# Kernel tuning notes

Measured on AMD Instinct MI355X. Metric: run time of the kernel, lower is better.

## Reference

```python
import jax, jax.numpy as jnp
import numpy as np
import math

D_MODEL = 1024
NUM_HEADS = 16
HEAD_DIM = D_MODEL // NUM_HEADS


def _xavier(key, out_f, in_f):
    limit = math.sqrt(6.0 / (in_f + out_f))
    return jax.random.uniform(key, (out_f, in_f), jnp.float32, -limit, limit)


def ternarize(w):
    # abs-mean threshold -> {-1, 0, +1}
    abs_mean = jnp.mean(jnp.abs(w))
    return jnp.where(jnp.abs(w) > abs_mean, jnp.sign(w), jnp.zeros_like(w))


def setup_inputs() -> dict:
    key = jax.random.key(0)
    kq, kk, kv, kwq, kwk, kwv, kwo = jax.random.split(key, 7)
    B, S = 2, 2048
    return {
        "query": jax.random.normal(kq, (B, S, D_MODEL), jnp.float32),
        "key": jax.random.normal(kk, (B, S, D_MODEL), jnp.float32),
        "value": jax.random.normal(kv, (B, S, D_MODEL), jnp.float32),
        "w_q": _xavier(kwq, D_MODEL, D_MODEL),
        "w_k": _xavier(kwk, D_MODEL, D_MODEL),
        "w_v": _xavier(kwv, D_MODEL, D_MODEL),
        "w_o": _xavier(kwo, D_MODEL, D_MODEL),
    }


def reference(query, key, value, w_q, w_k, w_v, w_o):
    B, S, _ = query.shape
    # ternary projections (F.linear: x @ W.T)
    q = query @ ternarize(w_q).T
    k = key @ ternarize(w_k).T
    v = value @ ternarize(w_v).T
    # [B, H, S, Dh]
    q = q.reshape(B, S, NUM_HEADS, HEAD_DIM).transpose(0, 2, 1, 3)
    k = k.reshape(B, -1, NUM_HEADS, HEAD_DIM).transpose(0, 2, 1, 3)
    v = v.reshape(B, -1, NUM_HEADS, HEAD_DIM).transpose(0, 2, 1, 3)
    scores = jnp.einsum("bhqd,bhkd->bhqk", q, k) / math.sqrt(HEAD_DIM)
    probs = jax.nn.softmax(scores, axis=-1)
    out = jnp.einsum("bhqk,bhkd->bhqd", probs, v)
    out = out.transpose(0, 2, 1, 3).reshape(B, S, D_MODEL)
    return out @ ternarize(w_o).T
```

## Files before the change

kernel.cpp:

```cpp
#include <hip/hip_runtime.h>
#include <cstdint>
#include <cstddef>

typedef __bf16 bfloat;
typedef __bf16 bf16x8 __attribute__((ext_vector_type(8)));
typedef __bf16 bf16x4 __attribute__((ext_vector_type(4)));
typedef float  f32x4  __attribute__((ext_vector_type(4)));

static constexpr int D  = 1024;
static constexpr int S  = 2048;
static constexpr int B  = 2;
static constexpr int H  = 16;
static constexpr int DH = 64;
static constexpr int M  = B * S;
static constexpr int WMAT_N = 1024 * 1024;

#define MFMA_BF16(a, b, c) __builtin_amdgcn_mfma_f32_16x16x32_bf16((a), (b), (c), 0, 0, 0)

__device__ __forceinline__ void gl_lds16(const void* g, void* l) {
  __builtin_amdgcn_global_load_lds(
      (const __attribute__((address_space(1))) void*)g,
      (__attribute__((address_space(3))) void*)l, 16, 0, 0);
}

__global__ void prep_kernel(const float* __restrict__ w0, const float* __restrict__ w1,
                            const float* __restrict__ w2, const float* __restrict__ w3,
                            double* __restrict__ sums) {
  const int y = blockIdx.y;
  const float* w = (y == 0) ? w0 : (y == 1) ? w1 : (y == 2) ? w2 : w3;
  const float4* w4 = (const float4*)w;
  double s = 0.0;
  for (int i = blockIdx.x * blockDim.x + threadIdx.x; i < (WMAT_N / 4);
       i += gridDim.x * blockDim.x) {
    float4 v = w4[i];
    s += (double)fabsf(v.x) + (double)fabsf(v.y) + (double)fabsf(v.z) + (double)fabsf(v.w);
  }
  for (int off = 1; off < 64; off <<= 1) s += __shfl_xor(s, off, 64);
  __shared__ double ps[4];
  if ((threadIdx.x & 63) == 0) ps[threadIdx.x >> 6] = s;
  __syncthreads();
  if (threadIdx.x == 0) atomicAdd(&sums[y], ps[0] + ps[1] + ps[2] + ps[3]);
}

__global__ void tern_kernel(const float* __restrict__ w0, const float* __restrict__ w1,
                            const float* __restrict__ w2, const float* __restrict__ w3,
                            bfloat* __restrict__ o0, bfloat* __restrict__ o1,
                            bfloat* __restrict__ o2, bfloat* __restrict__ o3,
                            const double* __restrict__ sums) {
  int z = blockIdx.y;
  const float* w = (z == 0) ? w0 : (z == 1) ? w1 : (z == 2) ? w2 : w3;
  bfloat* o = (z == 0) ? o0 : (z == 1) ? o1 : (z == 2) ? o2 : o3;
  double thr = sums[z] * (1.0 / (double)WMAT_N);
  const float4* w4 = (const float4*)w;
  for (int i = blockIdx.x * blockDim.x + threadIdx.x; i < (WMAT_N / 4);
       i += gridDim.x * blockDim.x) {
    float4 v = w4[i];
    bf16x4 r;
    r[0] = (bfloat)(((double)fabsf(v.x) > thr) ? (v.x > 0.f ? 1.f : -1.f) : 0.f);
    r[1] = (bfloat)(((double)fabsf(v.y) > thr) ? (v.y > 0.f ? 1.f : -1.f) : 0.f);
    r[2] = (bfloat)(((double)fabsf(v.z) > thr) ? (v.z > 0.f ? 1.f : -1.f) : 0.f);
    r[3] = (bfloat)(((double)fabsf(v.w) > thr) ? (v.w > 0.f ? 1.f : -1.f) : 0.f);
    *(bf16x4*)&o[(size_t)i * 4] = r;
  }
}

__global__ __launch_bounds__(256) void qkv_gemm(
    const float* __restrict__ xq, const float* __restrict__ xk,
    const float* __restrict__ xv, const bfloat* __restrict__ wqt,
    const bfloat* __restrict__ wkt, const bfloat* __restrict__ wvt,
    bfloat* __restrict__ qmh, bfloat* __restrict__ qml,
    bfloat* __restrict__ kmh, bfloat* __restrict__ kml, bfloat* __restrict__ vtr) {
  constexpr int K = D;
  constexpr int N = D;
  __shared__ __align__(16) bfloat As0[128 * 64];
  __shared__ __align__(16) bfloat As1[128 * 64];
  __shared__ __align__(16) bfloat Ws[128 * 64];

  const int bid = blockIdx.x;
  const int xcd = bid & 7;
  const int i6 = bid >> 3;
  const int slice = xcd * 12 + (i6 >> 3);
  const int bx = i6 & 7;
  const int z = slice >> 5;
  const int by = slice & 31;

  const float* Af;
  const bfloat* Wm;
  bfloat *Oh = nullptr, *Ol = nullptr;
  float scale = 1.f;
  bool split;
  if (z == 0) {
    Af = xq; Wm = wqt; Oh = qmh; Ol = qml;
    scale = 0.18033688f;
    split = true;
  } else if (z == 1) {
    Af = xk; Wm = wkt; Oh = kmh; Ol = kml; split = true;
  } else {
    Af = xv; Wm = wvt; split = false;
  }

  const int t = threadIdx.x;
  const int w = t >> 6, lane = t & 63;
  const int quad = lane >> 4, l16 = lane & 15;
  const int wm = w >> 1, wn = w & 1;
  const int m0 = by * 128, n0 = bx * 128;

  f32x4 acc[4][4] = {};

  const int srr = lane >> 3;
  const int spc = lane & 7;
  const int cl8 = (spc ^ srr) * 8;

  const float* aSrc[4];
#pragma unroll
  for (int g = 0; g < 4; g++)
    aSrc[g] = Af + (size_t)(m0 + w * 32 + g * 8 + srr) * K + cl8;

  float4 fa[4][2];
#pragma unroll
  for (int g = 0; g < 4; g++) {
    fa[g][0] = *(const float4*)(aSrc[g]);
    fa[g][1] = *(const float4*)(aSrc[g] + 4);
  }

  for (int kk = 0; kk < K; kk += 64) {
#pragma unroll
    for (int g = 0; g < 4; g++) {
      int rb = w * 32 + g * 8;
      gl_lds16(Wm + (size_t)(n0 + rb + srr) * K + kk + cl8, Ws + rb * 64);
    }
#pragma unroll
    for (int g = 0; g < 4; g++) {
      int row = w * 32 + g * 8 + srr;
      float f[8] = {fa[g][0].x, fa[g][0].y, fa[g][0].z, fa[g][0].w,
                    fa[g][1].x, fa[g][1].y, fa[g][1].z, fa[g][1].w};
      bf16x8 hh;
#pragma unroll
      for (int j = 0; j < 8; j++) hh[j] = (bfloat)f[j];
      const int da = row * 64 + spc * 8;
      *(bf16x8*)&As0[da] = hh;
      if (split) {
        bf16x8 ll;
#pragma unroll
        for (int j = 0; j < 8; j++) ll[j] = (bfloat)(f[j] - (float)hh[j]);
        *(bf16x8*)&As1[da] = ll;
      }
    }
    asm volatile("s_waitcnt vmcnt(0) lgkmcnt(0)" ::: "memory");
    __builtin_amdgcn_s_barrier();
    asm volatile("" ::: "memory");

    if (kk + 64 < K) {
#pragma unroll
      for (int g = 0; g < 4; g++) {
        fa[g][0] = *(const float4*)(aSrc[g] + kk + 64);
        fa[g][1] = *(const float4*)(aSrc[g] + kk + 64 + 4);
      }
    }

#pragma unroll
    for (int kidx = 0; kidx < 2; kidx++) {
      bf16x8 bfrag[4], afrag[4];
#pragma unroll
      for (int nt = 0; nt < 4; nt++) {
        int r = wn * 64 + nt * 16 + l16;
        bfrag[nt] = *(const bf16x8*)&Ws[r * 64 + (((kidx * 4 + quad) ^ (r & 7)) * 8)];
      }
#pragma unroll
      for (int mt = 0; mt < 4; mt++) {
        int r = wm * 64 + mt * 16 + l16;
        afrag[mt] = *(const bf16x8*)&As0[r * 64 + (((kidx * 4 + quad) ^ (r & 7)) * 8)];
      }
#pragma unroll
      for (int mt = 0; mt < 4; mt++)
#pragma unroll
        for (int nt = 0; nt < 4; nt++)
          acc[mt][nt] = MFMA_BF16(afrag[mt], bfrag[nt], acc[mt][nt]);
      if (split) {
#pragma unroll
        for (int mt = 0; mt < 4; mt++) {
          int r = wm * 64 + mt * 16 + l16;
          afrag[mt] = *(const bf16x8*)&As1[r * 64 + (((kidx * 4 + quad) ^ (r & 7)) * 8)];
        }
#pragma unroll
        for (int mt = 0; mt < 4; mt++)
#pragma unroll
          for (int nt = 0; nt < 4; nt++)
            acc[mt][nt] = MFMA_BF16(afrag[mt], bfrag[nt], acc[mt][nt]);
      }
    }
    asm volatile("" ::: "memory");
    __builtin_amdgcn_s_barrier();
    asm volatile("" ::: "memory");
  }

#pragma unroll
  for (int mt = 0; mt < 4; mt++) {
#pragma unroll
    for (int nt = 0; nt < 4; nt++) {
      const int row = m0 + wm * 64 + mt * 16 + quad * 4;
      const int col = n0 + wn * 64 + nt * 16 + l16;
      if (split) {
#pragma unroll
        for (int rg = 0; rg < 4; rg++) {
          float vv = acc[mt][nt][rg] * scale;
          size_t idx = (size_t)(row + rg) * N + col;
          bfloat hh = (bfloat)vv;
          Oh[idx] = hh;
          Ol[idx] = (bfloat)(vv - (float)hh);
        }
      } else {
        int bb = row >> 11, s = row & (S - 1);
        int kk6 = s & 63;
        int pos = (kk6 & 3) | (((kk6 >> 4) & 1) << 2) | (((kk6 >> 2) & 3) << 3) |
                  ((kk6 >> 5) << 5);
        int sp = (s & ~63) | pos;
        bf16x4 pk;
#pragma unroll
        for (int rg = 0; rg < 4; rg++) pk[rg] = (bfloat)acc[mt][nt][rg];
        *(bf16x4*)&vtr[(size_t)bb * D * S + (size_t)col * S + sp] = pk;
      }
    }
  }
}

__global__ __launch_bounds__(256) void gemm_wo(const bfloat* __restrict__ A,
                                               const bfloat* __restrict__ Wm,
                                               float* __restrict__ Cf) {
  constexpr int K = D;
  constexpr int N = D;
  __shared__ __align__(16) bfloat As[128 * 64];
  __shared__ __align__(16) bfloat Ws[64 * 64];

  const int bid = blockIdx.x;
  const int xcd = bid & 7;
  const int i6 = bid >> 3;
  const int by = xcd * 4 + (i6 >> 4);
  const int bx = i6 & 15;

  const int t = threadIdx.x;
  const int w = t >> 6, lane = t & 63;
  const int quad = lane >> 4, l16 = lane & 15;
  const int wm = w >> 1, wn = w & 1;
  const int m0 = by * 128, n0 = bx * 64;

  f32x4 acc[4][2] = {};

  const int srr = lane >> 3;
  const int spc = lane & 7;
  const int cl8 = (spc ^ srr) * 8;

  for (int kk = 0; kk < K; kk += 64) {
#pragma unroll
    for (int g = 0; g < 4; g++) {
      int rb = w * 32 + g * 8;
      gl_lds16(A + (size_t)(m0 + rb + srr) * K + kk + cl8, As + rb * 64);
    }
#pragma unroll
    for (int g = 0; g < 2; g++) {
      int rb = w * 16 + g * 8;
      gl_lds16(Wm + (size_t)(n0 + rb + srr) * K + kk + cl8, Ws + rb * 64);
    }
    __syncthreads();

#pragma unroll
    for (int kidx = 0; kidx < 2; kidx++) {
      bf16x8 af[4], bfr[2];
#pragma unroll
      for (int nt = 0; nt < 2; nt++) {
        int r = wn * 32 + nt * 16 + l16;
        bfr[nt] = *(const bf16x8*)&Ws[r * 64 + (((kidx * 4 + quad) ^ (r & 7)) * 8)];
      }
#pragma unroll
      for (int mt = 0; mt < 4; mt++) {
        int r = wm * 64 + mt * 16 + l16;
        af[mt] = *(const bf16x8*)&As[r * 64 + (((kidx * 4 + quad) ^ (r & 7)) * 8)];
      }
#pragma unroll
      for (int mt = 0; mt < 4; mt++)
#pragma unroll
        for (int nt = 0; nt < 2; nt++)
          acc[mt][nt] = MFMA_BF16(af[mt], bfr[nt], acc[mt][nt]);
    }
    __syncthreads();
  }

#pragma unroll
  for (int mt = 0; mt < 4; mt++) {
#pragma unroll
    for (int nt = 0; nt < 2; nt++) {
      const int row = m0 + wm * 64 + mt * 16 + quad * 4;
      const int col = n0 + wn * 32 + nt * 16 + l16;
#pragma unroll
      for (int rg = 0; rg < 4; rg++) Cf[(size_t)(row + rg) * N + col] = acc[mt][nt][rg];
    }
  }
}

__global__ __launch_bounds__(512) void flash_kernel(
    const bfloat* __restrict__ qh, const bfloat* __restrict__ ql,
    const bfloat* __restrict__ kh, const bfloat* __restrict__ kl,
    const bfloat* __restrict__ vt, bfloat* __restrict__ outp) {
  __shared__ __align__(16) bfloat SM[20480];

  const int tid = threadIdx.x;
  const int w = tid >> 6, lane = tid & 63;
  const int quad = lane >> 4, l16 = lane & 15;

  const int blk = blockIdx.x;
  const int xcd = blk & 7, slot = blk >> 3;
  const int g = xcd * 4 + (slot >> 4);
  const int h = g & 15, b = g >> 4;
  const int q0 = (slot & 15) * 128;

  const size_t base = (size_t)b * S * D + (size_t)h * DH;
  const size_t vbase = (size_t)b * D * S + (size_t)h * DH * S;

  const int ssr = lane >> 3;
  const int spc = lane & 7;
  const int c8 = (spc ^ ssr) * 8;
  const int stKV = w * 512;

  const bfloat* pKh = kh + base + (size_t)(w * 8 + ssr) * D + c8;
  const bfloat* pKl = kl + base + (size_t)(w * 8 + ssr) * D + c8;
  const bfloat* pV = vt + vbase + (size_t)(w * 8 + ssr) * S + c8;

  bf16x8 ones;
#pragma unroll
  for (int j = 0; j < 8; j++) ones[j] = (bfloat)1.f;

  {
    const bfloat* pQh = qh + base + (size_t)(q0 + w * 16 + ssr) * D + c8;
    const bfloat* pQl = ql + base + (size_t)(q0 + w * 16 + ssr) * D + c8;
    gl_lds16(pQh, SM + w * 1024);
    gl_lds16(pQh + 8 * D, SM + w * 1024 + 512);
    gl_lds16(pQl, SM + 8192 + w * 1024);
    gl_lds16(pQl + 8 * D, SM + 8192 + w * 1024 + 512);
  }
  asm volatile("s_waitcnt vmcnt(0)" ::: "memory");
  __builtin_amdgcn_s_barrier();
  asm volatile("" ::: "memory");

  const int fo0 = l16 * 64 + ((quad ^ (l16 & 7)) * 8);
  const int fo4 = fo0 ^ 32;
  const int fq = w * 1024;

  bf16x8 qhf0 = *(const bf16x8*)&SM[fq + fo0];
  bf16x8 qhf1 = *(const bf16x8*)&SM[fq + fo4];
  bf16x8 qlf0 = *(const bf16x8*)&SM[8192 + fq + fo0];
  bf16x8 qlf1 = *(const bf16x8*)&SM[8192 + fq + fo4];
  asm volatile("s_waitcnt lgkmcnt(0)" ::: "memory");
  __builtin_amdgcn_s_barrier();
  asm volatile("" ::: "memory");

  gl_lds16(pKh, SM + 0 + stKV);
  gl_lds16(pKl, SM + 4096 + stKV);
  pKh += 64 * D;
  pKl += 64 * D;
  asm volatile("s_waitcnt vmcnt(0)" ::: "memory");

  f32x4 Oa[4] = {};
  f32x4 La = {};
  float m_i = -3.0e38f;
  constexpr int NT = S / 64;

  for (int t = 0; t < NT; ++t) {
    __builtin_amdgcn_s_barrier();
    asm volatile("" ::: "memory");
    const int cur = (t & 1) * 8192;
    const int nxt = 8192 - cur;

    gl_lds16(pV, SM + 16384 + stKV);
    pV += 64;
    if (t < NT - 1) {
      gl_lds16(pKh, SM + nxt + stKV);
      gl_lds16(pKl, SM + nxt + 4096 + stKV);
      pKh += 64 * D;
      pKl += 64 * D;
    }

    f32x4 sf[4];
    __builtin_amdgcn_s_setprio(1);
#pragma unroll
    for (int mt = 0; mt < 4; mt++) {
      f32x4 a = {};
      bf16x8 bh0 = *(const bf16x8*)&SM[cur + fo0 + mt * 1024];
      bf16x8 bl0 = *(const bf16x8*)&SM[cur + 4096 + fo0 + mt * 1024];
      bf16x8 bh1 = *(const bf16x8*)&SM[cur + fo4 + mt * 1024];
      bf16x8 bl1 = *(const bf16x8*)&SM[cur + 4096 + fo4 + mt * 1024];
      a = MFMA_BF16(bh0, qhf0, a);
      a = MFMA_BF16(bl0, qhf0, a);
      a = MFMA_BF16(bh0, qlf0, a);
      a = MFMA_BF16(bh1, qhf1, a);
      a = MFMA_BF16(bl1, qhf1, a);
      a = MFMA_BF16(bh1, qlf1, a);
      sf[mt] = a;
    }
    __builtin_amdgcn_s_setprio(0);

    float t0 = fmaxf(fmaxf(sf[0][0], sf[0][1]), fmaxf(sf[0][2], sf[0][3]));
    float t1 = fmaxf(fmaxf(sf[1][0], sf[1][1]), fmaxf(sf[1][2], sf[1][3]));
    float t2 = fmaxf(fmaxf(sf[2][0], sf[2][1]), fmaxf(sf[2][2], sf[2][3]));
    float t3 = fmaxf(fmaxf(sf[3][0], sf[3][1]), fmaxf(sf[3][2], sf[3][3]));
    float mm = fmaxf(fmaxf(t0, t1), fmaxf(t2, t3));
    mm = fmaxf(mm, __shfl_xor(mm, 16, 64));
    mm = fmaxf(mm, __shfl_xor(mm, 32, 64));
    if (__ballot(mm > m_i + 8.0f)) {
      float mnew = fmaxf(m_i, mm);
      float alpha = exp2f(m_i - mnew);
      m_i = mnew;
#pragma unroll
      for (int mt = 0; mt < 4; mt++) Oa[mt] *= alpha;
      La *= alpha;
    }
#pragma unroll
    for (int mt = 0; mt < 4; mt++)
#pragma unroll
      for (int rg = 0; rg < 4; rg++) sf[mt][rg] = exp2f(sf[mt][rg] - m_i);

    if (t < NT - 1)
      asm volatile("s_waitcnt vmcnt(2)" ::: "memory");
    else
      asm volatile("s_waitcnt vmcnt(0)" ::: "memory");
    __builtin_amdgcn_s_barrier();
    asm volatile("" ::: "memory");

    __builtin_amdgcn_s_setprio(1);
#pragma unroll
    for (int kp = 0; kp < 2; kp++) {
      bf16x8 pb8;
#pragma unroll
      for (int rg = 0; rg < 4; rg++) {
        pb8[rg] = (bfloat)sf[2 * kp][rg];
        pb8[4 + rg] = (bfloat)sf[2 * kp + 1][rg];
      }
      La = MFMA_BF16(ones, pb8, La);
      const int fv = kp ? fo4 : fo0;
#pragma unroll
      for (int mt = 0; mt < 4; mt++) {
        bf16x8 va = *(const bf16x8*)&SM[16384 + fv + mt * 1024];
        Oa[mt] = MFMA_BF16(va, pb8, Oa[mt]);
      }
    }
    __builtin_amdgcn_s_setprio(0);
    asm volatile("s_waitcnt vmcnt(0)" ::: "memory");
  }

  float inv = 1.0f / La[0];
  const int qrow = q0 + w * 16 + l16;
#pragma unroll
  for (int mt = 0; mt < 4; mt++) {
    bf16x4 ov;
#pragma unroll
    for (int rg = 0; rg < 4; rg++) ov[rg] = (bfloat)(Oa[mt][rg] * inv);
    *(bf16x4*)&outp[base + (size_t)qrow * D + mt * 16 + quad * 4] = ov;
  }
}

extern "C" void kernel_launch(void* const* d_in, const int* in_sizes, int n_in,
                              void* d_out, int out_size, void* d_ws, size_t ws_size,
                              hipStream_t stream) {
  const float* q_in = (const float*)d_in[0];
  const float* k_in = (const float*)d_in[1];
  const float* v_in = (const float*)d_in[2];
  const float* wq = (const float*)d_in[3];
  const float* wk = (const float*)d_in[4];
  const float* wv = (const float*)d_in[5];
  const float* wo = (const float*)d_in[6];
  float* outp = (float*)d_out;
  char* ws = (char*)d_ws;

  constexpr size_t WBYTES = (size_t)WMAT_N * 2;
  constexpr size_t XBYTES = (size_t)M * D * 2;
  size_t off = 0;
  double* sums = (double*)(ws + off); off += 256;
  bfloat* wqt = (bfloat*)(ws + off); off += WBYTES;
  bfloat* wkt = (bfloat*)(ws + off); off += WBYTES;
  bfloat* wvt = (bfloat*)(ws + off); off += WBYTES;
  bfloat* wot = (bfloat*)(ws + off); off += WBYTES;
  bfloat* qmh = (bfloat*)(ws + off); off += XBYTES;
  bfloat* qml = (bfloat*)(ws + off); off += XBYTES;
  bfloat* kmh = (bfloat*)(ws + off); off += XBYTES;
  bfloat* kml = (bfloat*)(ws + off); off += XBYTES;
  bfloat* vtr = (bfloat*)(ws + off); off += XBYTES;
  bfloat* attn = (bfloat*)(ws + off); off += XBYTES;

  hipMemsetAsync(sums, 0, 4 * sizeof(double), stream);
  prep_kernel<<<dim3(256, 4), 256, 0, stream>>>(wq, wk, wv, wo, sums);
  tern_kernel<<<dim3(128, 4), 256, 0, stream>>>(wq, wk, wv, wo, wqt, wkt, wvt, wot, sums);
  qkv_gemm<<<768, 256, 0, stream>>>(
      q_in, k_in, v_in, wqt, wkt, wvt, qmh, qml, kmh, kml, vtr);
  flash_kernel<<<512, 512, 0, stream>>>(qmh, qml, kmh, kml, vtr, attn);
  gemm_wo<<<512, 256, 0, stream>>>(attn, wot, outp);
}
```

Baseline: 269.2 us.

## Load A fragments directly into registers and double-buffer weight tiles in LDS

The QKV projection GEMM no longer stages the fp32 activations through LDS as hi/lo bf16 tiles. Each lane now loads its MFMA A-fragment straight from global memory, converts it to hi/lo bf16 in registers, and prefetches the next k-step's fragment. The weight tile is double-buffered in LDS so the next tile's global-to-LDS load overlaps compute, which drops one barrier per iteration. In exchange the global A loads are less coalesced (per-lane 32-byte row chunks) and register pressure rises from holding two k-slices of fp32 prefetch.

```diff
diff --git a/kernel.cpp b/kernel.cpp
--- a/kernel.cpp
+++ b/kernel.cpp
@@ -72,9 +72,7 @@
     bfloat* __restrict__ kmh, bfloat* __restrict__ kml, bfloat* __restrict__ vtr) {
   constexpr int K = D;
   constexpr int N = D;
-  __shared__ __align__(16) bfloat As0[128 * 64];
-  __shared__ __align__(16) bfloat As1[128 * 64];
-  __shared__ __align__(16) bfloat Ws[128 * 64];
+  __shared__ __align__(16) bfloat Ws[2][128 * 64];
 
   const int bid = blockIdx.x;
   const int xcd = bid & 7;
@@ -111,87 +109,83 @@
   const int spc = lane & 7;
   const int cl8 = (spc ^ srr) * 8;
 
-  const float* aSrc[4];
+  const float* aB[4];
+#pragma unroll
+  for (int mt = 0; mt < 4; mt++)
+    aB[mt] = Af + (size_t)(m0 + wm * 64 + mt * 16 + l16) * K + quad * 8;
+
+  const bfloat* wB[4];
 #pragma unroll
   for (int g = 0; g < 4; g++)
-    aSrc[g] = Af + (size_t)(m0 + w * 32 + g * 8 + srr) * K + cl8;
-
-  float4 fa[4][2];
-#pragma unroll
-  for (int g = 0; g < 4; g++) {
-    fa[g][0] = *(const float4*)(aSrc[g]);
-    fa[g][1] = *(const float4*)(aSrc[g] + 4);
-  }
+    wB[g] = Wm + (size_t)(n0 + w * 32 + g * 8 + srr) * K + cl8;
+
+#pragma unroll
+  for (int g = 0; g < 4; g++) gl_lds16(wB[g], &Ws[0][(w * 32 + g * 8) * 64]);
+  float4 fa[4][2][2];
+#pragma unroll
+  for (int mt = 0; mt < 4; mt++)
+#pragma unroll
+    for (int kidx = 0; kidx < 2; kidx++) {
+      fa[mt][kidx][0] = *(const float4*)(aB[mt] + kidx * 32);
+      fa[mt][kidx][1] = *(const float4*)(aB[mt] + kidx * 32 + 4);
+    }
 
   for (int kk = 0; kk < K; kk += 64) {
-#pragma unroll
-    for (int g = 0; g < 4; g++) {
-      int rb = w * 32 + g * 8;
-      gl_lds16(Wm + (size_t)(n0 + rb + srr) * K + kk + cl8, Ws + rb * 64);
-    }
-#pragma unroll
-    for (int g = 0; g < 4; g++) {
-      int row = w * 32 + g * 8 + srr;
-      float f[8] = {fa[g][0].x, fa[g][0].y, fa[g][0].z, fa[g][0].w,
-                    fa[g][1].x, fa[g][1].y, fa[g][1].z, fa[g][1].w};
-      bf16x8 hh;
-#pragma unroll
-      for (int j = 0; j < 8; j++) hh[j] = (bfloat)f[j];
-      const int da = row * 64 + spc * 8;
-      *(bf16x8*)&As0[da] = hh;
-      if (split) {
-        bf16x8 ll;
-#pragma unroll
-        for (int j = 0; j < 8; j++) ll[j] = (bfloat)(f[j] - (float)hh[j]);
-        *(bf16x8*)&As1[da] = ll;
-      }
-    }
-    asm volatile("s_waitcnt vmcnt(0) lgkmcnt(0)" ::: "memory");
+    const int cur = (kk >> 6) & 1;
+    asm volatile("s_waitcnt vmcnt(0)" ::: "memory");
     __builtin_amdgcn_s_barrier();
     asm volatile("" ::: "memory");
 
     if (kk + 64 < K) {
 #pragma unroll
-      for (int g = 0; g < 4; g++) {
-        fa[g][0] = *(const float4*)(aSrc[g] + kk + 64);
-        fa[g][1] = *(const float4*)(aSrc[g] + kk + 64 + 4);
-      }
-    }
-
+      for (int g = 0; g < 4; g++)
+        gl_lds16(wB[g] + kk + 64, &Ws[1 - cur][(w * 32 + g * 8) * 64]);
+    }
+
+    const bfloat* wsc = &Ws[cur][0];
 #pragma unroll
     for (int kidx = 0; kidx < 2; kidx++) {
-      bf16x8 bfrag[4], afrag[4];
+      bf16x8 fh[4], fl[4];
+#pragma unroll
+      for (int mt = 0; mt < 4; mt++) {
+        float f[8] = {fa[mt][kidx][0].x, fa[mt][kidx][0].y, fa[mt][kidx][0].z,
+                      fa[mt][kidx][0].w, fa[mt][kidx][1].x, fa[mt][kidx][1].y,
+                      fa[mt][kidx][1].z, fa[mt][kidx][1].w};
+#pragma unroll
+        for (int j = 0; j < 8; j++) fh[mt][j] = (bfloat)f[j];
+        if (split) {
+#pragma unroll
+          for (int j = 0; j < 8; j++) fl[mt][j] = (bfloat)(f[j] - (float)fh[mt][j]);
+        }
+      }
+      if (kidx == 1 && kk + 64 < K) {
+#pragma unroll
+        for (int mt = 0; mt < 4; mt++)
+#pragma unroll
+          for (int kx = 0; kx < 2; kx++) {
+            fa[mt][kx][0] = *(const float4*)(aB[mt] + kk + 64 + kx * 32);
+            fa[mt][kx][1] = *(const float4*)(aB[mt] + kk + 64 + kx * 32 + 4);
+          }
+      }
+      bf16x8 bfrag[4];
 #pragma unroll
       for (int nt = 0; nt < 4; nt++) {
         int r = wn * 64 + nt * 16 + l16;
-        bfrag[nt] = *(const bf16x8*)&Ws[r * 64 + (((kidx * 4 + quad) ^ (r & 7)) * 8)];
-      }
-#pragma unroll
-      for (int mt = 0; mt < 4; mt++) {
-        int r = wm * 64 + mt * 16 + l16;
-        afrag[mt] = *(const bf16x8*)&As0[r * 64 + (((kidx * 4 + quad) ^ (r & 7)) * 8)];
+        bfrag[nt] = *(const bf16x8*)&wsc[r * 64 + (((kidx * 4 + quad) ^ (r & 7)) * 8)];
       }
 #pragma unroll
       for (int mt = 0; mt < 4; mt++)
 #pragma unroll
         for (int nt = 0; nt < 4; nt++)
-          acc[mt][nt] = MFMA_BF16(afrag[mt], bfrag[nt], acc[mt][nt]);
+          acc[mt][nt] = MFMA_BF16(fh[mt], bfrag[nt], acc[mt][nt]);
       if (split) {
 #pragma unroll
-        for (int mt = 0; mt < 4; mt++) {
-          int r = wm * 64 + mt * 16 + l16;
-          afrag[mt] = *(const bf16x8*)&As1[r * 64 + (((kidx * 4 + quad) ^ (r & 7)) * 8)];
-        }
-#pragma unroll
         for (int mt = 0; mt < 4; mt++)
 #pragma unroll
           for (int nt = 0; nt < 4; nt++)
-            acc[mt][nt] = MFMA_BF16(afrag[mt], bfrag[nt], acc[mt][nt]);
-      }
-    }
-    asm volatile("" ::: "memory");
-    __builtin_amdgcn_s_barrier();
-    asm volatile("" ::: "memory");
+            acc[mt][nt] = MFMA_BF16(fl[mt], bfrag[nt], acc[mt][nt]);
+      }
+    }
   }
 
 #pragma unroll
```

Result: slower. 345.4 us (+28.3%).
